# Performance work log

Measured on AMD Instinct MI355X. Metric: run time of the kernel, lower is better.

Reference implementation:

```python
import jax, jax.numpy as jnp
import numpy as np

V = 50257   # n_unique_words
C = 50257   # n_classes
E = 256     # embed_dim
H = 512     # h_dim
S_IN = 512
S_OUT = 511
START = 1


def setup_inputs() -> dict:
    key = jax.random.key(0)
    ks = jax.random.split(key, 12)
    s = 1.0 / np.sqrt(H)
    u = lambda k, shp: jax.random.uniform(k, shp, jnp.float32, -s, s)
    return {
        "h0": jnp.zeros((1, H), jnp.float32),
        "input_ids": jax.random.randint(ks[0], (1, S_IN), 0, V),
        "output_ids": jax.random.randint(ks[1], (1, S_OUT), 0, V),
        "emb": jax.random.normal(ks[2], (V, E), jnp.float32) * 0.02,
        "enc_wih": u(ks[3], (H, E)),
        "enc_whh": u(ks[4], (H, H)),
        "enc_bih": u(ks[5], (H,)),
        "enc_bhh": u(ks[5], (H,)),
        "dec_wih": u(ks[6], (H, E)),
        "dec_whh": u(ks[7], (H, H)),
        "dec_bih": u(ks[8], (H,)),
        "dec_bhh": u(ks[8], (H,)),
        "fc_w": u(ks[9], (C, H)),
        "fc_b": u(ks[10], (C,)),
    }


def _rnn_cell(x, h, wih, whh, bih, bhh):
    # Elman RNNCell: h' = tanh(x W_ih^T + b_ih + h W_hh^T + b_hh)
    return jnp.tanh(x @ wih.T + bih + h @ whh.T + bhh)


def reference(h0, input_ids, output_ids, emb, enc_wih, enc_whh, enc_bih, enc_bhh,
              dec_wih, dec_whh, dec_bih, dec_bhh, fc_w, fc_b):
    # ---- encode ----
    enc_xs = jnp.swapaxes(emb[input_ids], 0, 1)  # [S_in, 1, E]
    def enc_step(h, x):
        h = _rnn_cell(x, h, enc_wih, enc_whh, enc_bih, enc_bhh)
        return h, None
    hn, _ = jax.lax.scan(enc_step, h0, enc_xs)
    # ---- decode_train ----
    start_emb = emb[jnp.array([START])]          # [1, E]
    h1 = _rnn_cell(start_emb, hn, dec_wih, dec_whh, dec_bih, dec_bhh)
    dec_xs = jnp.swapaxes(emb[output_ids], 0, 1)  # [S_out, 1, E]
    def dec_step(h, x):
        h = _rnn_cell(x, h, dec_wih, dec_whh, dec_bih, dec_bhh)
        return h, h
    _, hs = jax.lax.scan(dec_step, h1, dec_xs)    # [S_out, 1, H]
    pred = jnp.concatenate([h1[None], hs], axis=0)[:, 0, :]  # [S_out+1, H]
    return pred @ fc_w.T + fc_b                   # [S_out+1, C]
```

## Files before the change

### kernel.cpp

```cpp
#include <hip/hip_runtime.h>
#include <hip/hip_fp16.h>

#define EDIM 256
#define HDIM 512
#define CDIM 50257

using half2_t = __attribute__((ext_vector_type(2))) _Float16;
using half8_t = __attribute__((ext_vector_type(8))) _Float16;
using float4_t = __attribute__((ext_vector_type(4))) float;

__device__ __forceinline__ float dot2(uint32_t w, uint32_t h, float acc) {
    return __builtin_amdgcn_fdot2(__builtin_bit_cast(half2_t, w),
                                  __builtin_bit_cast(half2_t, h), acc, false);
}

__device__ __forceinline__ float fast_tanh(float x) {
    float e = __builtin_amdgcn_exp2f(x * 2.8853900817779268f);
    return 1.f - 2.f * __builtin_amdgcn_rcpf(e + 1.f);
}

__global__ void __launch_bounds__(256) prep_ker(
    const float* __restrict__ enc_whh, const float* __restrict__ dec_whh,
    _Float16* __restrict__ wpe, _Float16* __restrict__ wpd,
    const float* __restrict__ fc_w, _Float16* __restrict__ fcw16,
    long fcw_n, int nb_cvt,
    const int* __restrict__ in_ids, const int* __restrict__ out_ids,
    const float* __restrict__ emb,
    const float* __restrict__ enc_wih, const float* __restrict__ enc_bih,
    const float* __restrict__ enc_bhh,
    const float* __restrict__ dec_wih, const float* __restrict__ dec_bih,
    const float* __restrict__ dec_bhh,
    float* __restrict__ z) {
    __shared__ float x[EDIM];
    int b = blockIdx.x;
    if (b < 256) {
        const float* whh = (b < 128) ? enc_whh : dec_whh;
        _Float16* wpack  = (b < 128) ? wpe : wpd;
        int idx = (b & 127) * 256 + threadIdx.x;
        int g = idx >> 9, t = idx & 511;
        int jr = g >> 2, i = g & 3;
        int row = ((t >> 4) << 4) + jr;
        int k0 = ((t & 15) << 5) + (i << 3);
        const float* src = whh + row * HDIM + k0;
        uint32_t d[4];
#pragma unroll
        for (int q = 0; q < 4; ++q) {
            half2_t p;
            p[0] = (_Float16)src[2 * q];
            p[1] = (_Float16)src[2 * q + 1];
            d[q] = __builtin_bit_cast(uint32_t, p);
        }
        ((uint4*)wpack)[g * 512 + t] = make_uint4(d[0], d[1], d[2], d[3]);
    } else if (b < 256 + nb_cvt) {
        long i = ((long)(b - 256) * 256 + threadIdx.x) * 8;
        if (i + 8 <= fcw_n) {
            const float4* s4 = (const float4*)(fc_w + i);
            float4 a = s4[0], bb = s4[1];
            half8_t o;
            o[0] = (_Float16)a.x;  o[1] = (_Float16)a.y;
            o[2] = (_Float16)a.z;  o[3] = (_Float16)a.w;
            o[4] = (_Float16)bb.x; o[5] = (_Float16)bb.y;
            o[6] = (_Float16)bb.z; o[7] = (_Float16)bb.w;
            *(half8_t*)(fcw16 + i) = o;
        }
    } else {
        int t = b - 256 - nb_cvt;
        const float *wih, *bih, *bhh;
        int id;
        if (t < 512) {
            wih = enc_wih; bih = enc_bih; bhh = enc_bhh; id = in_ids[t];
        } else {
            wih = dec_wih; bih = dec_bih; bhh = dec_bhh;
            id = (t == 512) ? 1 : out_ids[t - 513];
        }
        x[threadIdx.x] = emb[(long)id * EDIM + threadIdx.x];
        __syncthreads();
#pragma unroll
        for (int rr = 0; rr < 2; ++rr) {
            int r = threadIdx.x + rr * 256;
            const float4* w4 = (const float4*)(wih + r * EDIM);
            float acc = 0.f;
#pragma unroll 8
            for (int k4 = 0; k4 < 64; ++k4) {
                float4 wv = w4[k4];
                acc += wv.x * x[k4 * 4 + 0] + wv.y * x[k4 * 4 + 1] +
                       wv.z * x[k4 * 4 + 2] + wv.w * x[k4 * 4 + 3];
            }
            z[t * HDIM + r] = acc + bih[r] + bhh[r];
        }
    }
}

__global__ void __launch_bounds__(512, 2) scan_ker(
    const _Float16* __restrict__ wpack,
    const float* __restrict__ z,
    const _Float16* __restrict__ h_init,
    _Float16* __restrict__ hs_out,
    _Float16* __restrict__ hfin_out,
    int nsteps) {
    __shared__ uint4 wlds[16 * 512];
    __shared__ uint4 hbuf4[2][64];

    const int tid = threadIdx.x;
    const int c = tid & 15;
    const int g_own = tid >> 3;
    const int hstore = 128 * (g_own & 3) + 8 * (g_own >> 2) + (tid & 7);

    const uint4* wp4 = (const uint4*)wpack;
    uint32_t wreg[192];
#pragma unroll
    for (int g = 0; g < 48; ++g) {
        uint4 v = wp4[g * 512 + tid];
        wreg[g * 4 + 0] = v.x; wreg[g * 4 + 1] = v.y;
        wreg[g * 4 + 2] = v.z; wreg[g * 4 + 3] = v.w;
    }
#pragma unroll
    for (int g = 48; g < 64; ++g) wlds[(g - 48) * 512 + tid] = wp4[g * 512 + tid];

    ((_Float16*)hbuf4[0])[hstore] = h_init ? h_init[tid] : (_Float16)0.f;
    __syncthreads();

    _Float16 hlast = (_Float16)0.f;
    int cur = 0;
    for (int t = 0; t < nsteps; ++t) {
        float zv = z[t * HDIM + tid];
        const uint4* hb = hbuf4[cur];
        float acc[16];
#pragma unroll
        for (int r = 0; r < 16; ++r) acc[r] = 0.f;
#pragma unroll
        for (int i = 0; i < 4; ++i) {
            uint4 hg = hb[i * 16 + c];
#pragma unroll
            for (int jr = 0; jr < 12; ++jr) {
                acc[jr] = dot2(wreg[(jr * 4 + i) * 4 + 0], hg.x, acc[jr]);
                acc[jr] = dot2(wreg[(jr * 4 + i) * 4 + 1], hg.y, acc[jr]);
                acc[jr] = dot2(wreg[(jr * 4 + i) * 4 + 2], hg.z, acc[jr]);
                acc[jr] = dot2(wreg[(jr * 4 + i) * 4 + 3], hg.w, acc[jr]);
            }
#pragma unroll
            for (int js = 0; js < 4; ++js) {
                uint4 w = wlds[(js * 4 + i) * 512 + tid];
                acc[12 + js] = dot2(w.x, hg.x, acc[12 + js]);
                acc[12 + js] = dot2(w.y, hg.y, acc[12 + js]);
                acc[12 + js] = dot2(w.z, hg.z, acc[12 + js]);
                acc[12 + js] = dot2(w.w, hg.w, acc[12 + js]);
            }
        }
        float s, keep;
#define FOLD_DPP(aL, aH, bit, ctrl, dst)                                      \
        s = (c & bit) ? (aL) : (aH);                                          \
        s = __builtin_bit_cast(float, __builtin_amdgcn_mov_dpp(               \
                __builtin_bit_cast(int, s), ctrl, 0xF, 0xF, true));           \
        keep = (c & bit) ? (aH) : (aL);                                       \
        dst = keep + s;
#define FOLD_SWZ(aL, aH, bit, pat, dst)                                       \
        s = (c & bit) ? (aL) : (aH);                                          \
        s = __builtin_bit_cast(float, __builtin_amdgcn_ds_swizzle(            \
                __builtin_bit_cast(int, s), pat));                            \
        keep = (c & bit) ? (aH) : (aL);                                       \
        dst = keep + s;
        float b0, b1, b2, b3, b4, b5, b6, b7, d0, d1, d2, d3, e0, e1, v;
        FOLD_DPP(acc[0],  acc[1],  1, 0xB1, b0)
        FOLD_DPP(acc[2],  acc[3],  1, 0xB1, b1)
        FOLD_DPP(acc[4],  acc[5],  1, 0xB1, b2)
        FOLD_DPP(acc[6],  acc[7],  1, 0xB1, b3)
        FOLD_DPP(acc[8],  acc[9],  1, 0xB1, b4)
        FOLD_DPP(acc[10], acc[11], 1, 0xB1, b5)
        FOLD_DPP(acc[12], acc[13], 1, 0xB1, b6)
        FOLD_DPP(acc[14], acc[15], 1, 0xB1, b7)
        FOLD_DPP(b0, b1, 2, 0x4E, d0)
        FOLD_DPP(b2, b3, 2, 0x4E, d1)
        FOLD_DPP(b4, b5, 2, 0x4E, d2)
        FOLD_DPP(b6, b7, 2, 0x4E, d3)
        FOLD_DPP(d0, d2, 8, 0x128, e0)
        FOLD_DPP(d1, d3, 8, 0x128, e1)
        FOLD_SWZ(e0, e1, 4, 0x101F, v)
#undef FOLD_DPP
#undef FOLD_SWZ
        float hnew = fast_tanh(v + zv);
        _Float16 h16v = (_Float16)hnew;
        ((_Float16*)hbuf4[cur ^ 1])[hstore] = h16v;
        if (hs_out) hs_out[t * HDIM + tid] = h16v;
        hlast = h16v;
        __syncthreads();
        cur ^= 1;
    }
    if (hfin_out) hfin_out[tid] = hlast;
}

__global__ void __launch_bounds__(256) fc_ker16(const _Float16* __restrict__ A,
                                                const _Float16* __restrict__ Bw,
                                                const float* __restrict__ bias,
                                                float* __restrict__ out) {
    int n0 = blockIdx.x * 128, m0 = blockIdx.y * 128;
    int w = threadIdx.x >> 6, l = threadIdx.x & 63;
    int wm = (w >> 1) * 64, wn = (w & 1) * 64;
    int lr = l & 15, lk = (l >> 4) * 8;

    float4_t acc[4][4];
#pragma unroll
    for (int fm = 0; fm < 4; ++fm)
#pragma unroll
        for (int fn = 0; fn < 4; ++fn) acc[fm][fn] = (float4_t){0.f, 0.f, 0.f, 0.f};

    for (int ks = 0; ks < 512; ks += 32) {
        half8_t a[4], b[4];
#pragma unroll
        for (int f = 0; f < 4; ++f) {
            int m = m0 + wm + f * 16 + lr;
            a[f] = *(const half8_t*)(A + (long)m * 512 + ks + lk);
            int n = n0 + wn + f * 16 + lr;
            if (n < CDIM) {
                b[f] = *(const half8_t*)(Bw + (long)n * 512 + ks + lk);
            } else {
#pragma unroll
                for (int e = 0; e < 8; ++e) b[f][e] = (_Float16)0.f;
            }
        }
#pragma unroll
        for (int fm = 0; fm < 4; ++fm)
#pragma unroll
            for (int fn = 0; fn < 4; ++fn)
                acc[fm][fn] = __builtin_amdgcn_mfma_f32_16x16x32_f16(
                    a[fm], b[fn], acc[fm][fn], 0, 0, 0);
    }
#pragma unroll
    for (int fn = 0; fn < 4; ++fn) {
        int n = n0 + wn + fn * 16 + lr;
        if (n >= CDIM) continue;
        float bv = bias[n];
#pragma unroll
        for (int fm = 0; fm < 4; ++fm) {
#pragma unroll
            for (int q = 0; q < 4; ++q) {
                int m = m0 + wm + fm * 16 + (l >> 4) * 4 + q;
                out[(long)m * CDIM + n] = acc[fm][fn][q] + bv;
            }
        }
    }
}

__global__ void __launch_bounds__(256) fc_ker(const _Float16* __restrict__ A,
                                              const float* __restrict__ Bw,
                                              const float* __restrict__ bias,
                                              float* __restrict__ out) {
    int n0 = blockIdx.x * 128, m0 = blockIdx.y * 128;
    int w = threadIdx.x >> 6, l = threadIdx.x & 63;
    int wm = (w >> 1) * 64, wn = (w & 1) * 64;
    int lr = l & 15, lk = (l >> 4) * 8;

    float4_t acc[4][4];
#pragma unroll
    for (int fm = 0; fm < 4; ++fm)
#pragma unroll
        for (int fn = 0; fn < 4; ++fn) acc[fm][fn] = (float4_t){0.f, 0.f, 0.f, 0.f};

    for (int ks = 0; ks < 512; ks += 32) {
        half8_t a[4], b[4];
#pragma unroll
        for (int f = 0; f < 4; ++f) {
            int m = m0 + wm + f * 16 + lr;
            a[f] = *(const half8_t*)(A + (long)m * 512 + ks + lk);
            int n = n0 + wn + f * 16 + lr;
            half8_t bb;
            if (n < CDIM) {
                const float4* bp4 = (const float4*)(Bw + (long)n * 512 + ks + lk);
                float4 x0 = bp4[0], x1 = bp4[1];
                bb[0] = (_Float16)x0.x; bb[1] = (_Float16)x0.y;
                bb[2] = (_Float16)x0.z; bb[3] = (_Float16)x0.w;
                bb[4] = (_Float16)x1.x; bb[5] = (_Float16)x1.y;
                bb[6] = (_Float16)x1.z; bb[7] = (_Float16)x1.w;
            } else {
#pragma unroll
                for (int e = 0; e < 8; ++e) bb[e] = (_Float16)0.f;
            }
            b[f] = bb;
        }
#pragma unroll
        for (int fm = 0; fm < 4; ++fm)
#pragma unroll
            for (int fn = 0; fn < 4; ++fn)
                acc[fm][fn] = __builtin_amdgcn_mfma_f32_16x16x32_f16(
                    a[fm], b[fn], acc[fm][fn], 0, 0, 0);
    }
#pragma unroll
    for (int fn = 0; fn < 4; ++fn) {
        int n = n0 + wn + fn * 16 + lr;
        if (n >= CDIM) continue;
        float bv = bias[n];
#pragma unroll
        for (int fm = 0; fm < 4; ++fm) {
#pragma unroll
            for (int q = 0; q < 4; ++q) {
                int m = m0 + wm + fm * 16 + (l >> 4) * 4 + q;
                out[(long)m * CDIM + n] = acc[fm][fn][q] + bv;
            }
        }
    }
}

extern "C" void kernel_launch(void* const* d_in, const int* in_sizes, int n_in,
                              void* d_out, int out_size, void* d_ws, size_t ws_size,
                              hipStream_t stream) {
    const int* input_ids  = (const int*)d_in[1];
    const int* output_ids = (const int*)d_in[2];
    const float* emb      = (const float*)d_in[3];
    const float* enc_wih  = (const float*)d_in[4];
    const float* enc_whh  = (const float*)d_in[5];
    const float* enc_bih  = (const float*)d_in[6];
    const float* enc_bhh  = (const float*)d_in[7];
    const float* dec_wih  = (const float*)d_in[8];
    const float* dec_whh  = (const float*)d_in[9];
    const float* dec_bih  = (const float*)d_in[10];
    const float* dec_bhh  = (const float*)d_in[11];
    const float* fc_w     = (const float*)d_in[12];
    const float* fc_b     = (const float*)d_in[13];
    float* out = (float*)d_out;

    char* ws = (char*)d_ws;
    float* z        = (float*)ws;
    _Float16* wpe   = (_Float16*)(ws + (2u << 20));
    _Float16* wpd   = (_Float16*)(ws + (2u << 20) + (512u << 10));
    _Float16* h16   = (_Float16*)(ws + (3u << 20));
    _Float16* hn16  = (_Float16*)(ws + (3u << 20) + (512u << 10));
    _Float16* fcw16 = (_Float16*)(ws + (4u << 20));

    const long fcw_n = (long)CDIM * HDIM;
    bool use_f16_fc = ws_size >= (size_t)(4u << 20) + (size_t)fcw_n * 2;
    int nb_cvt = use_f16_fc ? (int)((fcw_n / 8 + 255) / 256) : 0;

    prep_ker<<<256 + nb_cvt + 1024, 256, 0, stream>>>(
        enc_whh, dec_whh, wpe, wpd,
        fc_w, fcw16, fcw_n, nb_cvt,
        input_ids, output_ids, emb,
        enc_wih, enc_bih, enc_bhh,
        dec_wih, dec_bih, dec_bhh, z);
    scan_ker<<<1, 512, 0, stream>>>(wpe, z, nullptr, nullptr, hn16, 512);
    scan_ker<<<1, 512, 0, stream>>>(wpd, z + 512 * HDIM, hn16, h16, nullptr, 512);
    if (use_f16_fc)
        fc_ker16<<<dim3((CDIM + 127) / 128, 4), 256, 0, stream>>>(h16, fcw16, fc_b, out);
    else
        fc_ker<<<dim3((CDIM + 127) / 128, 4), 256, 0, stream>>>(h16, fc_w, fc_b, out);
}
```

Before: 1.678 ms.

## Overlap decoder prep with encoder scan and stream FC behind decoder scan

Splits prep so that the decoder weight packing, decoder input projections and fc_w fp16 conversion run in the same launch as the encoder scan, on other blocks. The decoder scan and the FC GEMM are merged into one persistent kernel. Block 0 runs the recurrence and publishes a progress counter every 128 steps, while the other 255 blocks spin-wait on it and compute 128x256 output tiles as rows become ready. This hides the prep and FC time behind the serial scans, at the risk of spin-wait overhead and of deadlock if block 0 is not scheduled.

Result: faster. 1.641 ms (-2.2%).

```diff
diff --git a/kernel.cpp b/kernel.cpp
--- a/kernel.cpp
+++ b/kernel.cpp
@@ -4,6 +4,8 @@
 #define EDIM 256
 #define HDIM 512
 #define CDIM 50257
+#define NT_FC 197
+#define NJOBS (NT_FC * 4)
 
 using half2_t = __attribute__((ext_vector_type(2))) _Float16;
 using half8_t = __attribute__((ext_vector_type(8))) _Float16;
@@ -19,88 +21,11 @@
     return 1.f - 2.f * __builtin_amdgcn_rcpf(e + 1.f);
 }
 
-__global__ void __launch_bounds__(256) prep_ker(
-    const float* __restrict__ enc_whh, const float* __restrict__ dec_whh,
-    _Float16* __restrict__ wpe, _Float16* __restrict__ wpd,
-    const float* __restrict__ fc_w, _Float16* __restrict__ fcw16,
-    long fcw_n, int nb_cvt,
-    const int* __restrict__ in_ids, const int* __restrict__ out_ids,
-    const float* __restrict__ emb,
-    const float* __restrict__ enc_wih, const float* __restrict__ enc_bih,
-    const float* __restrict__ enc_bhh,
-    const float* __restrict__ dec_wih, const float* __restrict__ dec_bih,
-    const float* __restrict__ dec_bhh,
-    float* __restrict__ z) {
-    __shared__ float x[EDIM];
-    int b = blockIdx.x;
-    if (b < 256) {
-        const float* whh = (b < 128) ? enc_whh : dec_whh;
-        _Float16* wpack  = (b < 128) ? wpe : wpd;
-        int idx = (b & 127) * 256 + threadIdx.x;
-        int g = idx >> 9, t = idx & 511;
-        int jr = g >> 2, i = g & 3;
-        int row = ((t >> 4) << 4) + jr;
-        int k0 = ((t & 15) << 5) + (i << 3);
-        const float* src = whh + row * HDIM + k0;
-        uint32_t d[4];
-#pragma unroll
-        for (int q = 0; q < 4; ++q) {
-            half2_t p;
-            p[0] = (_Float16)src[2 * q];
-            p[1] = (_Float16)src[2 * q + 1];
-            d[q] = __builtin_bit_cast(uint32_t, p);
-        }
-        ((uint4*)wpack)[g * 512 + t] = make_uint4(d[0], d[1], d[2], d[3]);
-    } else if (b < 256 + nb_cvt) {
-        long i = ((long)(b - 256) * 256 + threadIdx.x) * 8;
-        if (i + 8 <= fcw_n) {
-            const float4* s4 = (const float4*)(fc_w + i);
-            float4 a = s4[0], bb = s4[1];
-            half8_t o;
-            o[0] = (_Float16)a.x;  o[1] = (_Float16)a.y;
-            o[2] = (_Float16)a.z;  o[3] = (_Float16)a.w;
-            o[4] = (_Float16)bb.x; o[5] = (_Float16)bb.y;
-            o[6] = (_Float16)bb.z; o[7] = (_Float16)bb.w;
-            *(half8_t*)(fcw16 + i) = o;
-        }
-    } else {
-        int t = b - 256 - nb_cvt;
-        const float *wih, *bih, *bhh;
-        int id;
-        if (t < 512) {
-            wih = enc_wih; bih = enc_bih; bhh = enc_bhh; id = in_ids[t];
-        } else {
-            wih = dec_wih; bih = dec_bih; bhh = dec_bhh;
-            id = (t == 512) ? 1 : out_ids[t - 513];
-        }
-        x[threadIdx.x] = emb[(long)id * EDIM + threadIdx.x];
-        __syncthreads();
-#pragma unroll
-        for (int rr = 0; rr < 2; ++rr) {
-            int r = threadIdx.x + rr * 256;
-            const float4* w4 = (const float4*)(wih + r * EDIM);
-            float acc = 0.f;
-#pragma unroll 8
-            for (int k4 = 0; k4 < 64; ++k4) {
-                float4 wv = w4[k4];
-                acc += wv.x * x[k4 * 4 + 0] + wv.y * x[k4 * 4 + 1] +
-                       wv.z * x[k4 * 4 + 2] + wv.w * x[k4 * 4 + 3];
-            }
-            z[t * HDIM + r] = acc + bih[r] + bhh[r];
-        }
-    }
-}
-
-__global__ void __launch_bounds__(512, 2) scan_ker(
-    const _Float16* __restrict__ wpack,
-    const float* __restrict__ z,
-    const _Float16* __restrict__ h_init,
-    _Float16* __restrict__ hs_out,
-    _Float16* __restrict__ hfin_out,
-    int nsteps) {
-    __shared__ uint4 wlds[16 * 512];
-    __shared__ uint4 hbuf4[2][64];
-
+__device__ __forceinline__ void scan_body(
+    const _Float16* __restrict__ wpack, const float* __restrict__ z,
+    const _Float16* __restrict__ h_init, _Float16* __restrict__ hs_out,
+    _Float16* __restrict__ hfin_out, int* prog, int nsteps,
+    uint4* wlds, uint4* hbuf4) {
     const int tid = threadIdx.x;
     const int c = tid & 15;
     const int g_own = tid >> 3;
@@ -117,14 +42,14 @@
 #pragma unroll
     for (int g = 48; g < 64; ++g) wlds[(g - 48) * 512 + tid] = wp4[g * 512 + tid];
 
-    ((_Float16*)hbuf4[0])[hstore] = h_init ? h_init[tid] : (_Float16)0.f;
+    ((_Float16*)hbuf4)[hstore] = h_init ? h_init[tid] : (_Float16)0.f;
     __syncthreads();
 
     _Float16 hlast = (_Float16)0.f;
     int cur = 0;
     for (int t = 0; t < nsteps; ++t) {
         float zv = z[t * HDIM + tid];
-        const uint4* hb = hbuf4[cur];
+        const uint4* hb = hbuf4 + cur * 64;
         float acc[16];
 #pragma unroll
         for (int r = 0; r < 16; ++r) acc[r] = 0.f;
@@ -180,121 +105,204 @@
 #undef FOLD_SWZ
         float hnew = fast_tanh(v + zv);
         _Float16 h16v = (_Float16)hnew;
-        ((_Float16*)hbuf4[cur ^ 1])[hstore] = h16v;
+        ((_Float16*)hbuf4)[(cur ^ 1) * 512 + hstore] = h16v;
         if (hs_out) hs_out[t * HDIM + tid] = h16v;
         hlast = h16v;
         __syncthreads();
+        if (prog && (t & 127) == 127 && tid == 0) {
+            __threadfence();
+            __hip_atomic_store(prog, t + 1, __ATOMIC_RELEASE,
+                               __HIP_MEMORY_SCOPE_AGENT);
+        }
         cur ^= 1;
     }
     if (hfin_out) hfin_out[tid] = hlast;
 }
 
-__global__ void __launch_bounds__(256) fc_ker16(const _Float16* __restrict__ A,
-                                                const _Float16* __restrict__ Bw,
-                                                const float* __restrict__ bias,
-                                                float* __restrict__ out) {
-    int n0 = blockIdx.x * 128, m0 = blockIdx.y * 128;
-    int w = threadIdx.x >> 6, l = threadIdx.x & 63;
-    int wm = (w >> 1) * 64, wn = (w & 1) * 64;
+__global__ void __launch_bounds__(256) prep_a(
+    const float* __restrict__ enc_whh, _Float16* __restrict__ wpe,
+    const int* __restrict__ in_ids, const float* __restrict__ emb,
+    const float* __restrict__ enc_wih, const float* __restrict__ enc_bih,
+    const float* __restrict__ enc_bhh, float* __restrict__ z,
+    int* __restrict__ prog) {
+    __shared__ float x[EDIM];
+    int b = blockIdx.x;
+    if (b == 0 && threadIdx.x == 0)
+        __hip_atomic_store(prog, 0, __ATOMIC_RELAXED, __HIP_MEMORY_SCOPE_AGENT);
+    if (b < 128) {
+        int idx = b * 256 + threadIdx.x;
+        int g = idx >> 9, t = idx & 511;
+        int jr = g >> 2, i = g & 3;
+        int row = ((t >> 4) << 4) + jr;
+        int k0 = ((t & 15) << 5) + (i << 3);
+        const float* src = enc_whh + row * HDIM + k0;
+        uint32_t d[4];
+#pragma unroll
+        for (int q = 0; q < 4; ++q) {
+            half2_t p;
+            p[0] = (_Float16)src[2 * q];
+            p[1] = (_Float16)src[2 * q + 1];
+            d[q] = __builtin_bit_cast(uint32_t, p);
+        }
+        ((uint4*)wpe)[g * 512 + t] = make_uint4(d[0], d[1], d[2], d[3]);
+    } else {
+        int t = b - 128;
+        int id = in_ids[t];
+        x[threadIdx.x] = emb[(long)id * EDIM + threadIdx.x];
+        __syncthreads();
+#pragma unroll
+        for (int rr = 0; rr < 2; ++rr) {
+            int r = threadIdx.x + rr * 256;
+            const float4* w4 = (const float4*)(enc_wih + r * EDIM);
+            float acc = 0.f;
+#pragma unroll 8
+            for (int k4 = 0; k4 < 64; ++k4) {
+                float4 wv = w4[k4];
+                acc += wv.x * x[k4 * 4 + 0] + wv.y * x[k4 * 4 + 1] +
+                       wv.z * x[k4 * 4 + 2] + wv.w * x[k4 * 4 + 3];
+            }
+            z[t * HDIM + r] = acc + enc_bih[r] + enc_bhh[r];
+        }
+    }
+}
+
+__global__ void __launch_bounds__(512, 2) enc_fused(
+    const _Float16* __restrict__ wpe, const float* __restrict__ z,
+    _Float16* __restrict__ hn16,
+    const float* __restrict__ dec_whh, _Float16* __restrict__ wpd,
+    const int* __restrict__ out_ids, const float* __restrict__ emb,
+    const float* __restrict__ dec_wih, const float* __restrict__ dec_bih,
+    const float* __restrict__ dec_bhh, float* __restrict__ zf,
+    const float* __restrict__ fc_w, _Float16* __restrict__ fcw16, long fcw_n) {
+    __shared__ uint4 wlds[16 * 512];
+    __shared__ uint4 hbuf4[2 * 64];
+    int b = blockIdx.x, tid = threadIdx.x;
+    if (b == 0) {
+        scan_body(wpe, z, nullptr, nullptr, hn16, nullptr, 512, wlds, hbuf4);
+    } else if (b < 65) {
+        int idx = (b - 1) * 512 + tid;
+        int g = idx >> 9, t = idx & 511;
+        int jr = g >> 2, i = g & 3;
+        int row = ((t >> 4) << 4) + jr;
+        int k0 = ((t & 15) << 5) + (i << 3);
+        const float* src = dec_whh + row * HDIM + k0;
+        uint32_t d[4];
+#pragma unroll
+        for (int q = 0; q < 4; ++q) {
+            half2_t p;
+            p[0] = (_Float16)src[2 * q];
+            p[1] = (_Float16)src[2 * q + 1];
+            d[q] = __builtin_bit_cast(uint32_t, p);
+        }
+        ((uint4*)wpd)[g * 512 + t] = make_uint4(d[0], d[1], d[2], d[3]);
+    } else if (b < 577) {
+        int t = 512 + (b - 65);
+        float* x = (float*)wlds;
+        int id = (t == 512) ? 1 : out_ids[t - 513];
+        if (tid < EDIM) x[tid] = emb[(long)id * EDIM + tid];
+        __syncthreads();
+        const float4* w4 = (const float4*)(dec_wih + tid * EDIM);
+        float acc = 0.f;
+#pragma unroll 8
+        for (int k4 = 0; k4 < 64; ++k4) {
+            float4 wv = w4[k4];
+            acc += wv.x * x[k4 * 4 + 0] + wv.y * x[k4 * 4 + 1] +
+                   wv.z * x[k4 * 4 + 2] + wv.w * x[k4 * 4 + 3];
+        }
+        zf[t * HDIM + tid] = acc + dec_bih[tid] + dec_bhh[tid];
+    } else {
+        long i = ((long)(b - 577) * 512 + tid) * 8;
+        if (i + 8 <= fcw_n) {
+            const float4* s4 = (const float4*)(fc_w + i);
+            float4 a = s4[0], bb = s4[1];
+            half8_t o;
+            o[0] = (_Float16)a.x;  o[1] = (_Float16)a.y;
+            o[2] = (_Float16)a.z;  o[3] = (_Float16)a.w;
+            o[4] = (_Float16)bb.x; o[5] = (_Float16)bb.y;
+            o[6] = (_Float16)bb.z; o[7] = (_Float16)bb.w;
+            *(half8_t*)(fcw16 + i) = o;
+        }
+    }
+}
+
+__global__ void __launch_bounds__(512, 2) dec_fc(
+    const _Float16* __restrict__ wpd, const float* __restrict__ zdec,
+    const _Float16* __restrict__ hn16, _Float16* __restrict__ h16,
+    int* __restrict__ prog,
+    const _Float16* __restrict__ Bw16, const float* __restrict__ Bw32,
+    int use16, const float* __restrict__ bias, float* __restrict__ out) {
+    __shared__ uint4 wlds[16 * 512];
+    __shared__ uint4 hbuf4[2 * 64];
+    int b = blockIdx.x, tid = threadIdx.x;
+    if (b == 0) {
+        scan_body(wpd, zdec, hn16, h16, nullptr, prog, 512, wlds, hbuf4);
+        return;
+    }
+    int w = tid >> 6, l = tid & 63;
+    int wm = (w >> 2) * 64, wn = (w & 3) * 64;
     int lr = l & 15, lk = (l >> 4) * 8;
-
-    float4_t acc[4][4];
-#pragma unroll
-    for (int fm = 0; fm < 4; ++fm)
-#pragma unroll
-        for (int fn = 0; fn < 4; ++fn) acc[fm][fn] = (float4_t){0.f, 0.f, 0.f, 0.f};
-
-    for (int ks = 0; ks < 512; ks += 32) {
-        half8_t a[4], b[4];
-#pragma unroll
-        for (int f = 0; f < 4; ++f) {
-            int m = m0 + wm + f * 16 + lr;
-            a[f] = *(const half8_t*)(A + (long)m * 512 + ks + lk);
-            int n = n0 + wn + f * 16 + lr;
-            if (n < CDIM) {
-                b[f] = *(const half8_t*)(Bw + (long)n * 512 + ks + lk);
-            } else {
-#pragma unroll
-                for (int e = 0; e < 8; ++e) b[f][e] = (_Float16)0.f;
-            }
-        }
+    for (int j = b - 1; j < NJOBS; j += 255) {
+        int mj = j / NT_FC, nj = j - mj * NT_FC;
+        if (tid == 0) {
+            int need = (mj + 1) * 128;
+            while (__hip_atomic_load(prog, __ATOMIC_ACQUIRE,
+                                     __HIP_MEMORY_SCOPE_AGENT) < need)
+                __builtin_amdgcn_s_sleep(16);
+            __threadfence();
+        }
+        __syncthreads();
+        int m0 = mj * 128, n0 = nj * 256;
+        float4_t acc[4][4];
 #pragma unroll
         for (int fm = 0; fm < 4; ++fm)
 #pragma unroll
             for (int fn = 0; fn < 4; ++fn)
-                acc[fm][fn] = __builtin_amdgcn_mfma_f32_16x16x32_f16(
-                    a[fm], b[fn], acc[fm][fn], 0, 0, 0);
-    }
-#pragma unroll
-    for (int fn = 0; fn < 4; ++fn) {
-        int n = n0 + wn + fn * 16 + lr;
-        if (n >= CDIM) continue;
-        float bv = bias[n];
-#pragma unroll
-        for (int fm = 0; fm < 4; ++fm) {
-#pragma unroll
-            for (int q = 0; q < 4; ++q) {
-                int m = m0 + wm + fm * 16 + (l >> 4) * 4 + q;
-                out[(long)m * CDIM + n] = acc[fm][fn][q] + bv;
-            }
-        }
-    }
-}
-
-__global__ void __launch_bounds__(256) fc_ker(const _Float16* __restrict__ A,
-                                              const float* __restrict__ Bw,
-                                              const float* __restrict__ bias,
-                                              float* __restrict__ out) {
-    int n0 = blockIdx.x * 128, m0 = blockIdx.y * 128;
-    int w = threadIdx.x >> 6, l = threadIdx.x & 63;
-    int wm = (w >> 1) * 64, wn = (w & 1) * 64;
-    int lr = l & 15, lk = (l >> 4) * 8;
-
-    float4_t acc[4][4];
-#pragma unroll
-    for (int fm = 0; fm < 4; ++fm)
-#pragma unroll
-        for (int fn = 0; fn < 4; ++fn) acc[fm][fn] = (float4_t){0.f, 0.f, 0.f, 0.f};
-
-    for (int ks = 0; ks < 512; ks += 32) {
-        half8_t a[4], b[4];
-#pragma unroll
-        for (int f = 0; f < 4; ++f) {
-            int m = m0 + wm + f * 16 + lr;
-            a[f] = *(const half8_t*)(A + (long)m * 512 + ks + lk);
-            int n = n0 + wn + f * 16 + lr;
-            half8_t bb;
-            if (n < CDIM) {
-                const float4* bp4 = (const float4*)(Bw + (long)n * 512 + ks + lk);
-                float4 x0 = bp4[0], x1 = bp4[1];
-                bb[0] = (_Float16)x0.x; bb[1] = (_Float16)x0.y;
-                bb[2] = (_Float16)x0.z; bb[3] = (_Float16)x0.w;
-                bb[4] = (_Float16)x1.x; bb[5] = (_Float16)x1.y;
-                bb[6] = (_Float16)x1.z; bb[7] = (_Float16)x1.w;
-            } else {
-#pragma unroll
-                for (int e = 0; e < 8; ++e) bb[e] = (_Float16)0.f;
-            }
-            b[f] = bb;
-        }
-#pragma unroll
-        for (int fm = 0; fm < 4; ++fm)
-#pragma unroll
-            for (int fn = 0; fn < 4; ++fn)
-                acc[fm][fn] = __builtin_amdgcn_mfma_f32_16x16x32_f16(
-                    a[fm], b[fn], acc[fm][fn], 0, 0, 0);
-    }
-#pragma unroll
-    for (int fn = 0; fn < 4; ++fn) {
-        int n = n0 + wn + fn * 16 + lr;
-        if (n >= CDIM) continue;
-        float bv = bias[n];
-#pragma unroll
-        for (int fm = 0; fm < 4; ++fm) {
-#pragma unroll
-            for (int q = 0; q < 4; ++q) {
-                int m = m0 + wm + fm * 16 + (l >> 4) * 4 + q;
-                out[(long)m * CDIM + n] = acc[fm][fn][q] + bv;
+                acc[fm][fn] = (float4_t){0.f, 0.f, 0.f, 0.f};
+        for (int ks = 0; ks < 512; ks += 32) {
+            half8_t a[4], bf[4];
+#pragma unroll
+            for (int f = 0; f < 4; ++f) {
+                int m = m0 + wm + f * 16 + lr;
+                a[f] = *(const half8_t*)(h16 + (long)m * 512 + ks + lk);
+                int n = n0 + wn + f * 16 + lr;
+                if (n < CDIM) {
+                    if (use16) {
+                        bf[f] = *(const half8_t*)(Bw16 + (long)n * 512 + ks + lk);
+                    } else {
+                        const float4* bp4 =
+                            (const float4*)(Bw32 + (long)n * 512 + ks + lk);
+                        float4 x0 = bp4[0], x1 = bp4[1];
+                        half8_t bb;
+                        bb[0] = (_Float16)x0.x; bb[1] = (_Float16)x0.y;
+                        bb[2] = (_Float16)x0.z; bb[3] = (_Float16)x0.w;
+                        bb[4] = (_Float16)x1.x; bb[5] = (_Float16)x1.y;
+                        bb[6] = (_Float16)x1.z; bb[7] = (_Float16)x1.w;
+                        bf[f] = bb;
+                    }
+                } else {
+#pragma unroll
+                    for (int e = 0; e < 8; ++e) bf[f][e] = (_Float16)0.f;
+                }
+            }
+#pragma unroll
+            for (int fm = 0; fm < 4; ++fm)
+#pragma unroll
+                for (int fn = 0; fn < 4; ++fn)
+                    acc[fm][fn] = __builtin_amdgcn_mfma_f32_16x16x32_f16(
+                        a[fm], bf[fn], acc[fm][fn], 0, 0, 0);
+        }
+#pragma unroll
+        for (int fn = 0; fn < 4; ++fn) {
+            int n = n0 + wn + fn * 16 + lr;
+            if (n >= CDIM) continue;
+            float bv = bias[n];
+#pragma unroll
+            for (int fm = 0; fm < 4; ++fm) {
+#pragma unroll
+                for (int q = 0; q < 4; ++q) {
+                    int m = m0 + wm + fm * 16 + (l >> 4) * 4 + q;
+                    out[(long)m * CDIM + n] = acc[fm][fn][q] + bv;
+                }
             }
         }
     }
@@ -324,22 +332,19 @@
     _Float16* wpd   = (_Float16*)(ws + (2u << 20) + (512u << 10));
     _Float16* h16   = (_Float16*)(ws + (3u << 20));
     _Float16* hn16  = (_Float16*)(ws + (3u << 20) + (512u << 10));
+    int* prog       = (int*)(ws + (3u << 20) + (513u << 10));
     _Float16* fcw16 = (_Float16*)(ws + (4u << 20));
 
     const long fcw_n = (long)CDIM * HDIM;
     bool use_f16_fc = ws_size >= (size_t)(4u << 20) + (size_t)fcw_n * 2;
-    int nb_cvt = use_f16_fc ? (int)((fcw_n / 8 + 255) / 256) : 0;
-
-    prep_ker<<<256 + nb_cvt + 1024, 256, 0, stream>>>(
-        enc_whh, dec_whh, wpe, wpd,
-        fc_w, fcw16, fcw_n, nb_cvt,
-        input_ids, output_ids, emb,
-        enc_wih, enc_bih, enc_bhh,
-        dec_wih, dec_bih, dec_bhh, z);
-    scan_ker<<<1, 512, 0, stream>>>(wpe, z, nullptr, nullptr, hn16, 512);
-    scan_ker<<<1, 512, 0, stream>>>(wpd, z + 512 * HDIM, hn16, h16, nullptr, 512);
-    if (use_f16_fc)
-        fc_ker16<<<dim3((CDIM + 127) / 128, 4), 256, 0, stream>>>(h16, fcw16, fc_b, out);
-    else
-        fc_ker<<<dim3((CDIM + 127) / 128, 4), 256, 0, stream>>>(h16, fc_w, fc_b, out);
-}
+    int nb_cvt = use_f16_fc ? (int)((fcw_n / 8 + 511) / 512) : 0;
+
+    prep_a<<<640, 256, 0, stream>>>(enc_whh, wpe, input_ids, emb,
+                                    enc_wih, enc_bih, enc_bhh, z, prog);
+    enc_fused<<<577 + nb_cvt, 512, 0, stream>>>(
+        wpe, z, hn16, dec_whh, wpd, output_ids, emb,
+        dec_wih, dec_bih, dec_bhh, z, fc_w, fcw16, fcw_n);
+    dec_fc<<<256, 512, 0, stream>>>(wpd, z + 512 * HDIM, hn16, h16, prog,
+                                    fcw16, fc_w, use_f16_fc ? 1 : 0,
+                                    fc_b, out);
+}
```
